# Optimization experiments

Hardware: AMD Instinct MI355X
Metric: run time of the kernel (lower is better)

The kernel has to match this reference:

```python
import jax, jax.numpy as jnp
import numpy as np

N = 50000      # num_nodes
F_IN = 128     # num_features
E = 800000     # num edges (before self-loops)
H1, D1 = 8, 16 # conv1: 8 heads x 16 dims -> 128 concat
D2 = 8         # conv2: 1 head x 8 dims
NEG_SLOPE = 0.2


def setup_inputs() -> dict:
    key = jax.random.key(0)
    ks = jax.random.split(key, 16)
    s = 0.05
    return {
        "x": jax.random.normal(ks[0], (N, F_IN), jnp.float32),
        "edge_index": jax.random.randint(ks[1], (2, E), 0, N, dtype=jnp.int64),
        "W1": jax.random.normal(ks[2], (F_IN, H1 * D1), jnp.float32) * s,
        "att_src1": jax.random.normal(ks[3], (H1, D1), jnp.float32) * s,
        "att_dst1": jax.random.normal(ks[4], (H1, D1), jnp.float32) * s,
        "b1": jnp.zeros((H1 * D1,), jnp.float32),
        "W2": jax.random.normal(ks[5], (H1 * D1, D2), jnp.float32) * s,
        "att_src2": jax.random.normal(ks[6], (1, D2), jnp.float32) * s,
        "att_dst2": jax.random.normal(ks[7], (1, D2), jnp.float32) * s,
        "b2": jnp.zeros((D2,), jnp.float32),
        "fc1_w": jax.random.normal(ks[8], (N * D2, 84), jnp.float32) * 0.005,
        "fc1_b": jnp.zeros((84,), jnp.float32),
        "fc2_w": jax.random.normal(ks[9], (84, 24), jnp.float32) * s,
        "fc2_b": jnp.zeros((24,), jnp.float32),
        "fc3_w": jax.random.normal(ks[10], (24, 2), jnp.float32) * s,
        "fc3_b": jnp.zeros((2,), jnp.float32),
    }


def gat_conv(x, src, dst, W, att_src, att_dst, bias, heads, out_dim):
    """PyG GATConv: per-head linear, edge attention, scatter-softmax over
    incoming edges per target node, weighted scatter-add aggregation."""
    n = x.shape[0]
    h = (x @ W).reshape(n, heads, out_dim)            # [N,H,D]
    a_src = jnp.einsum('nhd,hd->nh', h, att_src)      # [N,H]
    a_dst = jnp.einsum('nhd,hd->nh', h, att_dst)      # [N,H]
    e = jax.nn.leaky_relu(a_src[src] + a_dst[dst], NEG_SLOPE)  # [Et,H]
    # softmax over edges grouped by destination node (stable)
    m = jax.ops.segment_max(e, dst, num_segments=n)
    p = jnp.exp(e - m[dst])
    denom = jax.ops.segment_sum(p, dst, num_segments=n)
    alpha = p / denom[dst]                            # [Et,H]
    out = jax.ops.segment_sum(alpha[:, :, None] * h[src], dst, num_segments=n)
    return out.reshape(n, heads * out_dim) + bias


def reference(x, edge_index, W1, att_src1, att_dst1, b1,
              W2, att_src2, att_dst2, b2,
              fc1_w, fc1_b, fc2_w, fc2_b, fc3_w, fc3_b):
    # add self-loops (GATConv default add_self_loops=True)
    loop = jnp.arange(N, dtype=edge_index.dtype)
    src = jnp.concatenate([edge_index[0], loop])
    dst = jnp.concatenate([edge_index[1], loop])

    h = jax.nn.elu(gat_conv(x, src, dst, W1, att_src1, att_dst1, b1, H1, D1))
    h = jax.nn.elu(gat_conv(h, src, dst, W2, att_src2, att_dst2, b2, 1, D2))

    z = h.reshape(1, N * D2)                          # batch of one graph
    z = jax.nn.elu(z @ fc1_w + fc1_b)
    z = jax.nn.elu(z @ fc2_w + fc2_b)
    z = z @ fc3_w + fc3_b
    return jax.nn.log_softmax(z, axis=1)              # [1,2]
```

## Files before the change

### kernel.cpp

```cpp
#include <hip/hip_runtime.h>
#include <math.h>

#define N_NODES 50000
#define F_IN 128
#define NE 800000
#define NH1 8
#define ND1 16
#define ND2 8
#define NEG 0.2f
#define ZLEN (N_NODES * ND2)
#define NBLK 196
#define FC1_RPB 240
#define FC1_NB 1667

typedef __attribute__((ext_vector_type(8))) short bf16x8;
typedef __attribute__((ext_vector_type(4))) float f32x4;

__device__ __forceinline__ float lrelu(float v) { return v > 0.f ? v : NEG * v; }
__device__ __forceinline__ float elu1(float v)  { return v > 0.f ? v : (__expf(v) - 1.f); }

__device__ __forceinline__ unsigned short f2bf(float f) {
    union { float f; unsigned int i; } c; c.f = f;
    unsigned int u = c.i;
    return (unsigned short)((u + 0x7FFFu + ((u >> 16) & 1u)) >> 16);
}
__device__ __forceinline__ float bflo(unsigned int u) {
    union { unsigned int i; float f; } c; c.i = u << 16; return c.f;
}
__device__ __forceinline__ float bfhi(unsigned int u) {
    union { unsigned int i; float f; } c; c.i = u & 0xFFFF0000u; return c.f;
}
__device__ __forceinline__ int ei_is64(const int* __restrict__ ei) {
    return ((ei[1] | ei[3] | ei[5] | ei[7]) == 0) ? 1 : 0;
}

__global__ __launch_bounds__(256) void prep_kernel(const float* __restrict__ W,
                                                   uint4* __restrict__ wbf,
                                                   int* __restrict__ counts) {
    int i = blockIdx.x * 256 + threadIdx.x;
    if (i < N_NODES) counts[i] = 1;
    if (i < 2048) {
        int col = i >> 4, kc = i & 15;
        unsigned int u[4];
        #pragma unroll
        for (int jj = 0; jj < 4; ++jj) {
            unsigned int lo = f2bf(W[(kc * 8 + 2 * jj) * 128 + col]);
            unsigned int hi = f2bf(W[(kc * 8 + 2 * jj + 1) * 128 + col]);
            u[jj] = lo | (hi << 16);
        }
        uint4 v; v.x = u[0]; v.y = u[1]; v.z = u[2]; v.w = u[3];
        wbf[col * 16 + (kc ^ (col & 15))] = v;
    }
}

__global__ void hist_kernel(const int* __restrict__ ei, int* __restrict__ counts) {
    int e = blockIdx.x * blockDim.x + threadIdx.x;
    if (e >= NE) return;
    int is64 = ei_is64(ei);
    int d = is64 ? ei[2 * NE + 2 * e] : ei[NE + e];
    atomicAdd(&counts[d], 1);
}

__global__ __launch_bounds__(256) void scan1_kernel(const int* __restrict__ counts,
                                                    int* __restrict__ bsum) {
    const int t = threadIdx.x;
    int i = blockIdx.x * 256 + t;
    int v = (i < N_NODES) ? counts[i] : 0;
    #pragma unroll
    for (int off = 32; off; off >>= 1) v += __shfl_down(v, off, 64);
    __shared__ int ws[4];
    if ((t & 63) == 0) ws[t >> 6] = v;
    __syncthreads();
    if (t == 0) bsum[blockIdx.x] = ws[0] + ws[1] + ws[2] + ws[3];
}

__global__ __launch_bounds__(256) void scan2_kernel(const int* __restrict__ bsum,
                                                    int* __restrict__ boff) {
    const int t = threadIdx.x;
    const int lane = t & 63, w = t >> 6;
    int v = (t < NBLK) ? bsum[t] : 0;
    int incl = v;
    #pragma unroll
    for (int off = 1; off < 64; off <<= 1) {
        int u = __shfl_up(incl, off, 64);
        if (lane >= off) incl += u;
    }
    __shared__ int wsum[4];
    __shared__ int wpre[4];
    if (lane == 63) wsum[w] = incl;
    __syncthreads();
    if (t == 0) { int s = 0; for (int j = 0; j < 4; ++j) { wpre[j] = s; s += wsum[j]; } }
    __syncthreads();
    if (t < NBLK) boff[t] = incl - v + wpre[w];
}

__global__ __launch_bounds__(256) void scan3_kernel(const int* __restrict__ counts,
                                                    const int* __restrict__ boff,
                                                    int* __restrict__ rowptr,
                                                    int* __restrict__ cursor) {
    const int t = threadIdx.x;
    const int lane = t & 63, w = t >> 6;
    int i = blockIdx.x * 256 + t;
    int v = (i < N_NODES) ? counts[i] : 0;
    int incl = v;
    #pragma unroll
    for (int off = 1; off < 64; off <<= 1) {
        int u = __shfl_up(incl, off, 64);
        if (lane >= off) incl += u;
    }
    __shared__ int wsum[4];
    __shared__ int wpre[4];
    if (lane == 63) wsum[w] = incl;
    __syncthreads();
    if (t == 0) { int s = 0; for (int j = 0; j < 4; ++j) { wpre[j] = s; s += wsum[j]; } }
    __syncthreads();
    incl += wpre[w] + boff[blockIdx.x];
    if (i < N_NODES) { rowptr[i + 1] = incl; cursor[i] = incl - v; }
    if (i == 0) rowptr[0] = 0;
}

__global__ void fill_kernel(const int* __restrict__ ei,
                            int* __restrict__ cursor, int* __restrict__ esrc) {
    int i = blockIdx.x * blockDim.x + threadIdx.x;
    if (i >= NE + N_NODES) return;
    int s, d;
    if (i < NE) {
        int is64 = ei_is64(ei);
        if (is64) { s = ei[2 * i]; d = ei[2 * NE + 2 * i]; }
        else      { s = ei[i];     d = ei[NE + i]; }
    } else {
        s = d = i - NE;
    }
    int slot = atomicAdd(&cursor[d], 1);
    esrc[slot] = s;
}

__global__ __launch_bounds__(256) void gemm1_kernel(const float* __restrict__ x,
                                                    const uint4* __restrict__ wbf,
                                                    const float* __restrict__ att_src,
                                                    const float* __restrict__ att_dst,
                                                    unsigned int* __restrict__ h1b,
                                                    float* __restrict__ a_src1,
                                                    float* __restrict__ a_dst1) {
    __shared__ uint4 Xs[1024];
    __shared__ uint4 Ws[2048];
    const int t = threadIdx.x;
    const int row0 = blockIdx.x * 64;

    #pragma unroll
    for (int p = 0; p < 8; ++p) Ws[p * 256 + t] = wbf[p * 256 + t];

    #pragma unroll
    for (int p = 0; p < 4; ++p) {
        int cidx = p * 256 + t;
        int row = cidx >> 4, c = cidx & 15;
        int grow = row0 + row;
        float4 xa = make_float4(0.f, 0.f, 0.f, 0.f);
        float4 xb = make_float4(0.f, 0.f, 0.f, 0.f);
        if (grow < N_NODES) {
            xa = *reinterpret_cast<const float4*>(x + (size_t)grow * F_IN + c * 8);
            xb = *reinterpret_cast<const float4*>(x + (size_t)grow * F_IN + c * 8 + 4);
        }
        uint4 u;
        u.x = (unsigned int)f2bf(xa.x) | ((unsigned int)f2bf(xa.y) << 16);
        u.y = (unsigned int)f2bf(xa.z) | ((unsigned int)f2bf(xa.w) << 16);
        u.z = (unsigned int)f2bf(xb.x) | ((unsigned int)f2bf(xb.y) << 16);
        u.w = (unsigned int)f2bf(xb.z) | ((unsigned int)f2bf(xb.w) << 16);
        Xs[row * 16 + (c ^ (row & 15))] = u;
    }
    __syncthreads();

    const int wv = t >> 6;
    const int l  = t & 63;
    const int d  = l & 15;
    const int g  = l >> 4;
    const int arow = wv * 16 + d;

    f32x4 acc[8];
    #pragma unroll
    for (int n = 0; n < 8; ++n) { acc[n][0] = 0.f; acc[n][1] = 0.f; acc[n][2] = 0.f; acc[n][3] = 0.f; }

    #pragma unroll
    for (int ks = 0; ks < 4; ++ks) {
        int kc = ks * 4 + g;
        union { uint4 u; bf16x8 v; } A;
        A.u = Xs[arow * 16 + (kc ^ d)];
        #pragma unroll
        for (int n = 0; n < 8; ++n) {
            union { uint4 u; bf16x8 v; } B;
            B.u = Ws[(n * 16 + d) * 16 + (kc ^ d)];
            acc[n] = __builtin_amdgcn_mfma_f32_16x16x32_bf16(A.v, B.v, acc[n], 0, 0, 0);
        }
    }

    float as8[8], ad8[8];
    #pragma unroll
    for (int n = 0; n < 8; ++n) { as8[n] = att_src[n * 16 + d]; ad8[n] = att_dst[n * 16 + d]; }
    #pragma unroll
    for (int n = 0; n < 8; ++n) {
        #pragma unroll
        for (int r = 0; r < 4; ++r) {
            float ps = acc[n][r] * as8[n];
            float pd = acc[n][r] * ad8[n];
            #pragma unroll
            for (int off = 1; off < 16; off <<= 1) {
                ps += __shfl_xor(ps, off, 16);
                pd += __shfl_xor(pd, off, 16);
            }
            int grow = row0 + wv * 16 + g * 4 + r;
            if (d == 0 && grow < N_NODES) {
                a_src1[grow * 8 + n] = ps;
                a_dst1[grow * 8 + n] = pd;
            }
        }
    }
    #pragma unroll
    for (int n = 0; n < 8; ++n) {
        #pragma unroll
        for (int r = 0; r < 4; ++r) {
            float lo = acc[n][r];
            float hi = __shfl_xor(lo, 1, 64);
            int grow = row0 + wv * 16 + g * 4 + r;
            if (((d & 1) == 0) && grow < N_NODES) {
                unsigned int u = (unsigned int)f2bf(lo) | ((unsigned int)f2bf(hi) << 16);
                h1b[(size_t)grow * 64 + n * 8 + (d >> 1)] = u;
            }
        }
    }
}

__global__ __launch_bounds__(256) void agg1_kernel(const unsigned int* __restrict__ h1b,
                                                   const float* __restrict__ a_src,
                                                   const float* __restrict__ a_dst,
                                                   const int* __restrict__ rowptr,
                                                   const int* __restrict__ esrc,
                                                   const float* __restrict__ b1,
                                                   float* __restrict__ hout) {
    int wid = (blockIdx.x * 256 + threadIdx.x) >> 6;
    if (wid >= N_NODES) return;
    const int lane = threadIdx.x & 63;
    const int h = lane >> 3;
    const float ad = a_dst[wid * 8 + h];
    float acc0 = 0.f, acc1 = 0.f, den = 0.f;
    int j = rowptr[wid];
    const int jend = rowptr[wid + 1];
    for (; j + 8 <= jend; j += 8) {
        int s[8];
        #pragma unroll
        for (int k = 0; k < 8; ++k) s[k] = esrc[j + k];
        unsigned int u[8];
        #pragma unroll
        for (int k = 0; k < 8; ++k) u[k] = h1b[(size_t)s[k] * 64 + lane];
        float e[8];
        #pragma unroll
        for (int k = 0; k < 8; ++k) e[k] = a_src[s[k] * 8 + h];
        #pragma unroll
        for (int k = 0; k < 8; ++k) {
            float p = __expf(lrelu(e[k] + ad));
            den += p;
            acc0 = fmaf(p, bflo(u[k]), acc0);
            acc1 = fmaf(p, bfhi(u[k]), acc1);
        }
    }
    for (; j + 4 <= jend; j += 4) {
        int s0 = esrc[j], s1 = esrc[j + 1], s2 = esrc[j + 2], s3 = esrc[j + 3];
        unsigned int u0 = h1b[(size_t)s0 * 64 + lane];
        unsigned int u1 = h1b[(size_t)s1 * 64 + lane];
        unsigned int u2 = h1b[(size_t)s2 * 64 + lane];
        unsigned int u3 = h1b[(size_t)s3 * 64 + lane];
        float e0 = a_src[s0 * 8 + h], e1 = a_src[s1 * 8 + h];
        float e2 = a_src[s2 * 8 + h], e3 = a_src[s3 * 8 + h];
        float p0 = __expf(lrelu(e0 + ad));
        float p1 = __expf(lrelu(e1 + ad));
        float p2 = __expf(lrelu(e2 + ad));
        float p3 = __expf(lrelu(e3 + ad));
        den += (p0 + p1) + (p2 + p3);
        acc0 = fmaf(p0, bflo(u0), acc0); acc1 = fmaf(p0, bfhi(u0), acc1);
        acc0 = fmaf(p1, bflo(u1), acc0); acc1 = fmaf(p1, bfhi(u1), acc1);
        acc0 = fmaf(p2, bflo(u2), acc0); acc1 = fmaf(p2, bfhi(u2), acc1);
        acc0 = fmaf(p3, bflo(u3), acc0); acc1 = fmaf(p3, bfhi(u3), acc1);
    }
    for (; j < jend; ++j) {
        int s = esrc[j];
        unsigned int u = h1b[(size_t)s * 64 + lane];
        float e = a_src[s * 8 + h];
        float p = __expf(lrelu(e + ad));
        den += p;
        acc0 = fmaf(p, bflo(u), acc0);
        acc1 = fmaf(p, bfhi(u), acc1);
    }
    float inv = 1.f / den;
    float2 bb = *reinterpret_cast<const float2*>(b1 + 2 * lane);
    float o0 = elu1(acc0 * inv + bb.x);
    float o1 = elu1(acc1 * inv + bb.y);
    *reinterpret_cast<float2*>(hout + (size_t)wid * F_IN + 2 * lane) = make_float2(o0, o1);
}

__global__ __launch_bounds__(256) void gemm2_kernel(const float* __restrict__ h,
                                                    const float* __restrict__ W2,
                                                    const float* __restrict__ att_src2,
                                                    const float* __restrict__ att_dst2,
                                                    float* __restrict__ h2,
                                                    float* __restrict__ a_src2,
                                                    float* __restrict__ a_dst2) {
    __shared__ float Ws[F_IN * ND2];
    __shared__ float Hs[32 * 132];
    int t = threadIdx.x;
    int node0 = blockIdx.x * 32;
    #pragma unroll
    for (int i = 0; i < 4; ++i) { int idx = i * 256 + t; Ws[idx] = W2[idx]; }
    #pragma unroll
    for (int i = 0; i < 4; ++i) {
        int fidx = i * 256 + t;
        int r = fidx >> 5;
        int c4 = fidx & 31;
        int grow = node0 + r;
        float4 v = make_float4(0.f, 0.f, 0.f, 0.f);
        if (grow < N_NODES) v = *reinterpret_cast<const float4*>(h + (size_t)grow * F_IN + c4 * 4);
        *reinterpret_cast<float4*>(&Hs[r * 132 + c4 * 4]) = v;
    }
    __syncthreads();
    int nsub = t >> 3, d = t & 7;
    int node = node0 + nsub;
    float acc = 0.f;
    #pragma unroll 8
    for (int k = 0; k < F_IN; ++k)
        acc = fmaf(Hs[nsub * 132 + k], Ws[k * ND2 + d], acc);
    float vs = acc * att_src2[d];
    float vd = acc * att_dst2[d];
    #pragma unroll
    for (int off = 4; off >= 1; off >>= 1) {
        vs += __shfl_xor(vs, off, 8);
        vd += __shfl_xor(vd, off, 8);
    }
    if (node < N_NODES) {
        h2[node * ND2 + d] = acc;
        if (d == 0) { a_src2[node] = vs; a_dst2[node] = vd; }
    }
}

__global__ void agg2_kernel(const float* __restrict__ h2,
                            const float* __restrict__ a_src2, const float* __restrict__ a_dst2,
                            const int* __restrict__ rowptr, const int* __restrict__ esrc,
                            const float* __restrict__ b2, float* __restrict__ g) {
    int n = blockIdx.x * blockDim.x + threadIdx.x;
    if (n >= N_NODES) return;
    float ad = a_dst2[n];
    float acc[8] = {0.f, 0.f, 0.f, 0.f, 0.f, 0.f, 0.f, 0.f};
    float den = 0.f;
    int jend = rowptr[n + 1];
    for (int j = rowptr[n]; j < jend; ++j) {
        int s = esrc[j];
        float p = __expf(lrelu(a_src2[s] + ad));
        den += p;
        float4 va = *reinterpret_cast<const float4*>(h2 + s * ND2);
        float4 vb = *reinterpret_cast<const float4*>(h2 + s * ND2 + 4);
        acc[0] = fmaf(p, va.x, acc[0]); acc[1] = fmaf(p, va.y, acc[1]);
        acc[2] = fmaf(p, va.z, acc[2]); acc[3] = fmaf(p, va.w, acc[3]);
        acc[4] = fmaf(p, vb.x, acc[4]); acc[5] = fmaf(p, vb.y, acc[5]);
        acc[6] = fmaf(p, vb.z, acc[6]); acc[7] = fmaf(p, vb.w, acc[7]);
    }
    float inv = 1.f / den;
    float4 o0 = make_float4(elu1(acc[0] * inv + b2[0]), elu1(acc[1] * inv + b2[1]),
                            elu1(acc[2] * inv + b2[2]), elu1(acc[3] * inv + b2[3]));
    float4 o1 = make_float4(elu1(acc[4] * inv + b2[4]), elu1(acc[5] * inv + b2[5]),
                            elu1(acc[6] * inv + b2[6]), elu1(acc[7] * inv + b2[7]));
    *reinterpret_cast<float4*>(g + n * ND2)     = o0;
    *reinterpret_cast<float4*>(g + n * ND2 + 4) = o1;
}

__global__ __launch_bounds__(256) void fc1_stage1(const float* __restrict__ z,
                                                  const float* __restrict__ w,
                                                  float* __restrict__ partial) {
    __shared__ float zs[FC1_RPB];
    __shared__ float4 red[252];
    const int t = threadIdx.x;
    const int b = blockIdx.x;
    const int r0 = b * FC1_RPB;
    if (t < FC1_RPB) {
        int gr = r0 + t;
        zs[t] = (gr < ZLEN) ? z[gr] : 0.f;
    }
    __syncthreads();
    const int c4 = t % 21;
    const int rr = t / 21;
    if (t < 252) {
        float4 a = make_float4(0.f, 0.f, 0.f, 0.f);
        const float4* __restrict__ w4 = reinterpret_cast<const float4*>(w);
        if (r0 + FC1_RPB <= ZLEN) {
            #pragma unroll
            for (int bq = 0; bq < 5; ++bq) {
                float4 wv[4];
                float  zv[4];
                #pragma unroll
                for (int u = 0; u < 4; ++u) {
                    int i = bq * 48 + u * 12 + rr;
                    wv[u] = w4[(size_t)(r0 + i) * 21 + c4];
                    zv[u] = zs[i];
                }
                #pragma unroll
                for (int u = 0; u < 4; ++u) {
                    a.x = fmaf(zv[u], wv[u].x, a.x);
                    a.y = fmaf(zv[u], wv[u].y, a.y);
                    a.z = fmaf(zv[u], wv[u].z, a.z);
                    a.w = fmaf(zv[u], wv[u].w, a.w);
                }
            }
        } else {
            for (int i = rr; i < FC1_RPB; i += 12) {
                if (r0 + i < ZLEN) {
                    float4 wv = w4[(size_t)(r0 + i) * 21 + c4];
                    float  zv = zs[i];
                    a.x = fmaf(zv, wv.x, a.x); a.y = fmaf(zv, wv.y, a.y);
                    a.z = fmaf(zv, wv.z, a.z); a.w = fmaf(zv, wv.w, a.w);
                }
            }
        }
        red[t] = a;
    }
    __syncthreads();
    if (t < 21) {
        float4 s = red[t];
        #pragma unroll
        for (int k = 1; k < 12; ++k) {
            float4 v = red[k * 21 + t];
            s.x += v.x; s.y += v.y; s.z += v.z; s.w += v.w;
        }
        *reinterpret_cast<float4*>(partial + (size_t)b * 88 + t * 4) = s;
    }
}

__global__ __launch_bounds__(1024) void fctail_kernel(const float* __restrict__ partial,
                                                      const float* __restrict__ fc1_b,
                                                      const float* __restrict__ fc2_w,
                                                      const float* __restrict__ fc2_b,
                                                      const float* __restrict__ fc3_w,
                                                      const float* __restrict__ fc3_b,
                                                      float* __restrict__ out) {
    __shared__ float red[1008];
    __shared__ float z1[84];
    __shared__ float z2[24];
    const int t = threadIdx.x;
    if (t < 1008) {
        const int j  = t % 84;
        const int sl = t / 84;
        float s = 0.f;
        for (int b = sl; b < FC1_NB; b += 12)
            s += partial[(size_t)b * 88 + j];
        red[t] = s;
    }
    __syncthreads();
    if (t < 84) {
        float s = 0.f;
        #pragma unroll
        for (int sl = 0; sl < 12; ++sl) s += red[sl * 84 + t];
        z1[t] = elu1(s + fc1_b[t]);
    }
    __syncthreads();
    if (t < 24) {
        float a = fc2_b[t];
        for (int i = 0; i < 84; ++i) a = fmaf(z1[i], fc2_w[i * 24 + t], a);
        z2[t] = elu1(a);
    }
    __syncthreads();
    if (t == 0) {
        float z3[2];
        #pragma unroll
        for (int jj = 0; jj < 2; ++jj) {
            float a = fc3_b[jj];
            for (int i = 0; i < 24; ++i) a = fmaf(z2[i], fc3_w[i * 2 + jj], a);
            z3[jj] = a;
        }
        float m = fmaxf(z3[0], z3[1]);
        float l = m + logf(__expf(z3[0] - m) + __expf(z3[1] - m));
        out[0] = z3[0] - l;
        out[1] = z3[1] - l;
    }
}

extern "C" void kernel_launch(void* const* d_in, const int* in_sizes, int n_in,
                              void* d_out, int out_size, void* d_ws, size_t ws_size,
                              hipStream_t stream) {
    const float* x        = (const float*)d_in[0];
    const int*   ei       = (const int*)d_in[1];
    const float* W1       = (const float*)d_in[2];
    const float* att_src1 = (const float*)d_in[3];
    const float* att_dst1 = (const float*)d_in[4];
    const float* b1       = (const float*)d_in[5];
    const float* W2       = (const float*)d_in[6];
    const float* att_src2 = (const float*)d_in[7];
    const float* att_dst2 = (const float*)d_in[8];
    const float* b2       = (const float*)d_in[9];
    const float* fc1_w    = (const float*)d_in[10];
    const float* fc1_b    = (const float*)d_in[11];
    const float* fc2_w    = (const float*)d_in[12];
    const float* fc2_b    = (const float*)d_in[13];
    const float* fc3_w    = (const float*)d_in[14];
    const float* fc3_b    = (const float*)d_in[15];
    float* out = (float*)d_out;

    char* ws = (char*)d_ws;
    unsigned int* h1b = (unsigned int*)(ws + 0);
    float* hbuf   = (float*)(ws + 12800000);
    float* a_src1 = (float*)(ws + 38400000);
    float* a_dst1 = (float*)(ws + 40000000);
    float* h2     = (float*)(ws + 41600000);
    float* a_src2 = (float*)(ws + 43200000);
    float* a_dst2 = (float*)(ws + 43400000);
    float* g      = (float*)(ws + 43600000);
    int*   counts = (int*)  (ws + 45200000);
    int*   rowptr = (int*)  (ws + 45400000);
    int*   cursor = (int*)  (ws + 45600064);
    int*   esrc   = (int*)  (ws + 45800064);
    float* partial= (float*)(ws + 49200064);
    uint4* wbf    = (uint4*)(ws + 49786848);
    int*   bsum   = (int*)  (ws + 49819616);
    int*   boff   = (int*)  (ws + 49820400);

    prep_kernel<<<NBLK, 256, 0, stream>>>(W1, wbf, counts);
    hist_kernel<<<(NE + 255) / 256, 256, 0, stream>>>(ei, counts);
    scan1_kernel<<<NBLK, 256, 0, stream>>>(counts, bsum);
    scan2_kernel<<<1, 256, 0, stream>>>(bsum, boff);
    scan3_kernel<<<NBLK, 256, 0, stream>>>(counts, boff, rowptr, cursor);
    fill_kernel<<<(NE + N_NODES + 255) / 256, 256, 0, stream>>>(ei, cursor, esrc);

    gemm1_kernel<<<(N_NODES + 63) / 64, 256, 0, stream>>>(x, wbf, att_src1, att_dst1, h1b, a_src1, a_dst1);
    agg1_kernel<<<(N_NODES + 3) / 4, 256, 0, stream>>>(h1b, a_src1, a_dst1, rowptr, esrc, b1, hbuf);

    gemm2_kernel<<<(N_NODES + 31) / 32, 256, 0, stream>>>(hbuf, W2, att_src2, att_dst2, h2, a_src2, a_dst2);
    agg2_kernel<<<(N_NODES + 255) / 256, 256, 0, stream>>>(h2, a_src2, a_dst2, rowptr, esrc, b2, g);

    fc1_stage1<<<FC1_NB, 256, 0, stream>>>(g, fc1_w, partial);
    fctail_kernel<<<1, 1024, 0, stream>>>(partial, fc1_b, fc2_w, fc2_b, fc3_w, fc3_b, out);
}
```

Baseline: 256.5 us.

## Fuse layer-2 linear projection into agg1 and vectorize edge-index reads

The second GAT layer's 128x8 projection and attention logits are now computed inside agg1 with wave-wide shuffle reductions. This removes the gemm2 kernel and the 25.6 MB fp32 round trip of the intermediate hidden buffer. Separately, the histogram and CSR fill kernels each process four edges per thread using int4 loads. The cost is 48 extra cross-lane shuffles per node in agg1 and more atomics per thread.

```diff
diff --git a/kernel.cpp b/kernel.cpp
--- a/kernel.cpp
+++ b/kernel.cpp
@@ -54,11 +54,22 @@
 }
 
 __global__ void hist_kernel(const int* __restrict__ ei, int* __restrict__ counts) {
-    int e = blockIdx.x * blockDim.x + threadIdx.x;
-    if (e >= NE) return;
-    int is64 = ei_is64(ei);
-    int d = is64 ? ei[2 * NE + 2 * e] : ei[NE + e];
-    atomicAdd(&counts[d], 1);
+    int t = blockIdx.x * blockDim.x + threadIdx.x;
+    if (t * 4 >= NE) return;
+    int d0, d1, d2, d3;
+    if (ei_is64(ei)) {
+        const int4* p = reinterpret_cast<const int4*>(ei + 2 * NE);
+        int4 a = p[t * 2];
+        int4 b = p[t * 2 + 1];
+        d0 = a.x; d1 = a.z; d2 = b.x; d3 = b.z;
+    } else {
+        int4 a = reinterpret_cast<const int4*>(ei + NE)[t];
+        d0 = a.x; d1 = a.y; d2 = a.z; d3 = a.w;
+    }
+    atomicAdd(&counts[d0], 1);
+    atomicAdd(&counts[d1], 1);
+    atomicAdd(&counts[d2], 1);
+    atomicAdd(&counts[d3], 1);
 }
 
 __global__ __launch_bounds__(256) void scan1_kernel(const int* __restrict__ counts,
@@ -121,18 +132,31 @@
 
 __global__ void fill_kernel(const int* __restrict__ ei,
                             int* __restrict__ cursor, int* __restrict__ esrc) {
-    int i = blockIdx.x * blockDim.x + threadIdx.x;
-    if (i >= NE + N_NODES) return;
-    int s, d;
-    if (i < NE) {
-        int is64 = ei_is64(ei);
-        if (is64) { s = ei[2 * i]; d = ei[2 * NE + 2 * i]; }
-        else      { s = ei[i];     d = ei[NE + i]; }
+    const int t = blockIdx.x * blockDim.x + threadIdx.x;
+    const int NT_E = NE / 4;
+    if (t < NT_E) {
+        int s0, s1, s2, s3, d0, d1, d2, d3;
+        if (ei_is64(ei)) {
+            const int4* ps = reinterpret_cast<const int4*>(ei);
+            const int4* pd = reinterpret_cast<const int4*>(ei + 2 * NE);
+            int4 sa = ps[t * 2], sb = ps[t * 2 + 1];
+            int4 da = pd[t * 2], db = pd[t * 2 + 1];
+            s0 = sa.x; s1 = sa.z; s2 = sb.x; s3 = sb.z;
+            d0 = da.x; d1 = da.z; d2 = db.x; d3 = db.z;
+        } else {
+            int4 sa = reinterpret_cast<const int4*>(ei)[t];
+            int4 da = reinterpret_cast<const int4*>(ei + NE)[t];
+            s0 = sa.x; s1 = sa.y; s2 = sa.z; s3 = sa.w;
+            d0 = da.x; d1 = da.y; d2 = da.z; d3 = da.w;
+        }
+        esrc[atomicAdd(&cursor[d0], 1)] = s0;
+        esrc[atomicAdd(&cursor[d1], 1)] = s1;
+        esrc[atomicAdd(&cursor[d2], 1)] = s2;
+        esrc[atomicAdd(&cursor[d3], 1)] = s3;
     } else {
-        s = d = i - NE;
-    }
-    int slot = atomicAdd(&cursor[d], 1);
-    esrc[slot] = s;
+        int i = t - NT_E;
+        if (i < N_NODES) esrc[atomicAdd(&cursor[i], 1)] = i;
+    }
 }
 
 __global__ __launch_bounds__(256) void gemm1_kernel(const float* __restrict__ x,
@@ -235,12 +259,22 @@
                                                    const int* __restrict__ rowptr,
                                                    const int* __restrict__ esrc,
                                                    const float* __restrict__ b1,
-                                                   float* __restrict__ hout) {
+                                                   const float* __restrict__ W2,
+                                                   const float* __restrict__ att_src2,
+                                                   const float* __restrict__ att_dst2,
+                                                   float* __restrict__ h2,
+                                                   float* __restrict__ a_src2,
+                                                   float* __restrict__ a_dst2) {
     int wid = (blockIdx.x * 256 + threadIdx.x) >> 6;
     if (wid >= N_NODES) return;
     const int lane = threadIdx.x & 63;
     const int h = lane >> 3;
     const float ad = a_dst[wid * 8 + h];
+    float4 w2a0 = *reinterpret_cast<const float4*>(W2 + (2 * lane) * 8);
+    float4 w2a1 = *reinterpret_cast<const float4*>(W2 + (2 * lane) * 8 + 4);
+    float4 w2b0 = *reinterpret_cast<const float4*>(W2 + (2 * lane + 1) * 8);
+    float4 w2b1 = *reinterpret_cast<const float4*>(W2 + (2 * lane + 1) * 8 + 4);
+
     float acc0 = 0.f, acc1 = 0.f, den = 0.f;
     int j = rowptr[wid];
     const int jend = rowptr[wid + 1];
@@ -293,49 +327,33 @@
     float2 bb = *reinterpret_cast<const float2*>(b1 + 2 * lane);
     float o0 = elu1(acc0 * inv + bb.x);
     float o1 = elu1(acc1 * inv + bb.y);
-    *reinterpret_cast<float2*>(hout + (size_t)wid * F_IN + 2 * lane) = make_float2(o0, o1);
-}
-
-__global__ __launch_bounds__(256) void gemm2_kernel(const float* __restrict__ h,
-                                                    const float* __restrict__ W2,
-                                                    const float* __restrict__ att_src2,
-                                                    const float* __restrict__ att_dst2,
-                                                    float* __restrict__ h2,
-                                                    float* __restrict__ a_src2,
-                                                    float* __restrict__ a_dst2) {
-    __shared__ float Ws[F_IN * ND2];
-    __shared__ float Hs[32 * 132];
-    int t = threadIdx.x;
-    int node0 = blockIdx.x * 32;
-    #pragma unroll
-    for (int i = 0; i < 4; ++i) { int idx = i * 256 + t; Ws[idx] = W2[idx]; }
-    #pragma unroll
-    for (int i = 0; i < 4; ++i) {
-        int fidx = i * 256 + t;
-        int r = fidx >> 5;
-        int c4 = fidx & 31;
-        int grow = node0 + r;
-        float4 v = make_float4(0.f, 0.f, 0.f, 0.f);
-        if (grow < N_NODES) v = *reinterpret_cast<const float4*>(h + (size_t)grow * F_IN + c4 * 4);
-        *reinterpret_cast<float4*>(&Hs[r * 132 + c4 * 4]) = v;
-    }
-    __syncthreads();
-    int nsub = t >> 3, d = t & 7;
-    int node = node0 + nsub;
-    float acc = 0.f;
-    #pragma unroll 8
-    for (int k = 0; k < F_IN; ++k)
-        acc = fmaf(Hs[nsub * 132 + k], Ws[k * ND2 + d], acc);
-    float vs = acc * att_src2[d];
-    float vd = acc * att_dst2[d];
-    #pragma unroll
-    for (int off = 4; off >= 1; off >>= 1) {
-        vs += __shfl_xor(vs, off, 8);
-        vd += __shfl_xor(vd, off, 8);
-    }
-    if (node < N_NODES) {
-        h2[node * ND2 + d] = acc;
-        if (d == 0) { a_src2[node] = vs; a_dst2[node] = vd; }
+
+    float pd[8];
+    pd[0] = o0 * w2a0.x + o1 * w2b0.x;
+    pd[1] = o0 * w2a0.y + o1 * w2b0.y;
+    pd[2] = o0 * w2a0.z + o1 * w2b0.z;
+    pd[3] = o0 * w2a0.w + o1 * w2b0.w;
+    pd[4] = o0 * w2a1.x + o1 * w2b1.x;
+    pd[5] = o0 * w2a1.y + o1 * w2b1.y;
+    pd[6] = o0 * w2a1.z + o1 * w2b1.z;
+    pd[7] = o0 * w2a1.w + o1 * w2b1.w;
+    #pragma unroll
+    for (int dd = 0; dd < 8; ++dd) {
+        #pragma unroll
+        for (int off = 1; off < 64; off <<= 1)
+            pd[dd] += __shfl_xor(pd[dd], off, 64);
+    }
+    if (lane == 0) {
+        *reinterpret_cast<float4*>(h2 + wid * 8)     = make_float4(pd[0], pd[1], pd[2], pd[3]);
+        *reinterpret_cast<float4*>(h2 + wid * 8 + 4) = make_float4(pd[4], pd[5], pd[6], pd[7]);
+        float vs = 0.f, vd = 0.f;
+        #pragma unroll
+        for (int dd = 0; dd < 8; ++dd) {
+            vs = fmaf(pd[dd], att_src2[dd], vs);
+            vd = fmaf(pd[dd], att_dst2[dd], vd);
+        }
+        a_src2[wid] = vs;
+        a_dst2[wid] = vd;
     }
 }
 
@@ -501,33 +519,32 @@
 
     char* ws = (char*)d_ws;
     unsigned int* h1b = (unsigned int*)(ws + 0);
-    float* hbuf   = (float*)(ws + 12800000);
-    float* a_src1 = (float*)(ws + 38400000);
-    float* a_dst1 = (float*)(ws + 40000000);
-    float* h2     = (float*)(ws + 41600000);
-    float* a_src2 = (float*)(ws + 43200000);
-    float* a_dst2 = (float*)(ws + 43400000);
-    float* g      = (float*)(ws + 43600000);
-    int*   counts = (int*)  (ws + 45200000);
-    int*   rowptr = (int*)  (ws + 45400000);
-    int*   cursor = (int*)  (ws + 45600064);
-    int*   esrc   = (int*)  (ws + 45800064);
-    float* partial= (float*)(ws + 49200064);
-    uint4* wbf    = (uint4*)(ws + 49786848);
-    int*   bsum   = (int*)  (ws + 49819616);
-    int*   boff   = (int*)  (ws + 49820400);
+    float* a_src1 = (float*)(ws + 12800000);
+    float* a_dst1 = (float*)(ws + 14400000);
+    float* h2     = (float*)(ws + 16000000);
+    float* a_src2 = (float*)(ws + 17600000);
+    float* a_dst2 = (float*)(ws + 17800000);
+    float* g      = (float*)(ws + 18000000);
+    int*   counts = (int*)  (ws + 19600000);
+    int*   rowptr = (int*)  (ws + 19800000);
+    int*   cursor = (int*)  (ws + 20000064);
+    int*   esrc   = (int*)  (ws + 20200064);
+    float* partial= (float*)(ws + 23600064);
+    uint4* wbf    = (uint4*)(ws + 24186848);
+    int*   bsum   = (int*)  (ws + 24219616);
+    int*   boff   = (int*)  (ws + 24220400);
 
     prep_kernel<<<NBLK, 256, 0, stream>>>(W1, wbf, counts);
-    hist_kernel<<<(NE + 255) / 256, 256, 0, stream>>>(ei, counts);
+    hist_kernel<<<(NE / 4 + 255) / 256, 256, 0, stream>>>(ei, counts);
     scan1_kernel<<<NBLK, 256, 0, stream>>>(counts, bsum);
     scan2_kernel<<<1, 256, 0, stream>>>(bsum, boff);
     scan3_kernel<<<NBLK, 256, 0, stream>>>(counts, boff, rowptr, cursor);
-    fill_kernel<<<(NE + N_NODES + 255) / 256, 256, 0, stream>>>(ei, cursor, esrc);
+    fill_kernel<<<(NE / 4 + N_NODES + 255) / 256, 256, 0, stream>>>(ei, cursor, esrc);
 
     gemm1_kernel<<<(N_NODES + 63) / 64, 256, 0, stream>>>(x, wbf, att_src1, att_dst1, h1b, a_src1, a_dst1);
-    agg1_kernel<<<(N_NODES + 3) / 4, 256, 0, stream>>>(h1b, a_src1, a_dst1, rowptr, esrc, b1, hbuf);
-
-    gemm2_kernel<<<(N_NODES + 31) / 32, 256, 0, stream>>>(hbuf, W2, att_src2, att_dst2, h2, a_src2, a_dst2);
+    agg1_kernel<<<(N_NODES + 3) / 4, 256, 0, stream>>>(h1b, a_src1, a_dst1, rowptr, esrc, b1,
+                                                       W2, att_src2, att_dst2, h2, a_src2, a_dst2);
+
     agg2_kernel<<<(N_NODES + 255) / 256, 256, 0, stream>>>(h2, a_src2, a_dst2, rowptr, esrc, b2, g);
 
     fc1_stage1<<<FC1_NB, 256, 0, stream>>>(g, fc1_w, partial);
```

Result: slower. 266.0 us (+3.7%).
